# Performance work log

Measured on AMD Instinct MI355X. Metric: run time of the kernel, lower is better.

The kernel has to match this reference:

```python
import jax, jax.numpy as jnp
import numpy as np

GAMMA = 0.05
EPS = 1e-12
H, NH, HD = 768, 12, 64

def _lin(x, W, b):
    return x @ W.T + b

def _pproc(x, W, b):
    # LRP gamma-rule projection: forward value equals _lin(x, W, b); gradient flows through the gamma-modified layer times a detached ratio.
    z = _lin(x, W, b)
    zp = _lin(x, W + GAMMA * jnp.clip(W, 0.0, None), b + GAMMA * jnp.clip(b, 0.0, None))
    return zp * jax.lax.stop_gradient(z / zp)

def setup_inputs() -> dict:
    key = jax.random.key(0)
    ks = jax.random.split(key, 9)
    s = 0.02
    d = {"hidden_states": jax.random.normal(ks[0], (2, 2048, H), jnp.float32)}
    for i, n in enumerate(["q", "k", "v", "o"]):
        d["W" + n] = jax.random.normal(ks[1 + 2 * i], (H, H), jnp.float32) * s
        d["b" + n] = jax.random.normal(ks[2 + 2 * i], (H,), jnp.float32) * s
    return d

def reference(hidden_states, Wq, bq, Wk, bk, Wv, bv, Wo, bo):
    B, S, _ = hidden_states.shape
    def heads(x):  # [B,S,H] -> [B,NH,S,HD]
        return x.reshape(B, S, NH, HD).transpose(0, 2, 1, 3)
    q = heads(_pproc(hidden_states, Wq, bq))
    k = heads(_pproc(hidden_states, Wk, bk))
    v = heads(_pproc(hidden_states, Wv, bv))
    # NOTE: source has NO 1/sqrt(d_head) scaling on the scores
    scores = jnp.einsum("bhsd,bhtd->bhst", q, k)
    probs = jax.lax.stop_gradient(jax.nn.softmax(scores, axis=-1))  # detach_kq branch
    ctx = jnp.einsum("bhst,bhtd->bhsd", probs, v).transpose(0, 2, 1, 3).reshape(B, S, H)
    # BertSelfOutput.pforward: gamma-modified dense applied directly (no pproc ratio)
    pWo = Wo + GAMMA * jnp.clip(Wo, 0.0, None)
    pbo = bo + GAMMA * jnp.clip(bo, 0.0, None)
    y = _lin(ctx, pWo, pbo) + hidden_states
    # 'nowb' LayerNorm with detached mean and std (torch.std -> unbiased, ddof=1)
    mean = jax.lax.stop_gradient(jnp.mean(y, axis=-1, keepdims=True))
    std = jax.lax.stop_gradient(jnp.std(y, axis=-1, keepdims=True, ddof=1))
    out = (y - mean) / (std + EPS)
    return out, probs
```

## Files before the change

kernel.cpp:

```cpp
#include <hip/hip_runtime.h>

#define GAMMA 0.05f
#define LNEPS 1e-12f
#define HDIMT 768
#define SDIM  2048
#define NHEAD 12
#define HDHEAD 64
#define MTOT  4096
#define BHEADS 24
#define OUT0E ((size_t)MTOT * HDIMT)
#define NXEL  ((size_t)MTOT * HDIMT)
#define WNEL  ((size_t)HDIMT * HDIMT)
#define NEATT ((size_t)BHEADS * SDIM * HDHEAD)

typedef __attribute__((ext_vector_type(8))) short short8;
typedef __attribute__((ext_vector_type(4))) float f32x4;

#define MFMA16(a, b, c) __builtin_amdgcn_mfma_f32_16x16x32_bf16((a), (b), (c), 0, 0, 0)

__device__ __forceinline__ float bf2f(unsigned short u) {
    union { unsigned int i; float f; } c; c.i = ((unsigned int)u) << 16; return c.f;
}
__device__ __forceinline__ unsigned short f2bf(float f) {
    union { float f; unsigned int i; } c; c.f = f;
    unsigned int i = c.i;
    i += 0x7FFFu + ((i >> 16) & 1u);
    return (unsigned short)(i >> 16);
}
__device__ __forceinline__ void splitbf(float v, unsigned short& h, unsigned short& l) {
    h = f2bf(v);
    l = f2bf(v - bf2f(h));
}

__device__ __forceinline__ void load8f(const void* p, size_t idx, int isbf, float* r) {
    if (isbf) {
        const unsigned short* b = (const unsigned short*)p + idx;
        uint4 u = *(const uint4*)b;
        const unsigned short* pu = (const unsigned short*)&u;
        #pragma unroll
        for (int j = 0; j < 8; ++j) r[j] = bf2f(pu[j]);
    } else {
        const float* f = (const float*)p + idx;
        float4 a = *(const float4*)f, c = *(const float4*)(f + 4);
        r[0] = a.x; r[1] = a.y; r[2] = a.z; r[3] = a.w;
        r[4] = c.x; r[5] = c.y; r[6] = c.z; r[7] = c.w;
    }
}
__device__ __forceinline__ float load1f(const void* p, size_t idx, int isbf) {
    return isbf ? bf2f(((const unsigned short*)p)[idx]) : ((const float*)p)[idx];
}

__global__ void detect_kernel(const void* __restrict__ x, int* __restrict__ flag) {
    __shared__ int cnt;
    if (threadIdx.x == 0) cnt = 0;
    __syncthreads();
    const unsigned short* u = (const unsigned short*)x;
    unsigned short v = u[2 * threadIdx.x];
    int e = (v >> 7) & 0xFF;
    int ok = (e >= 100 && e <= 140) ? 1 : 0;
    atomicAdd(&cnt, ok);
    __syncthreads();
    if (threadIdx.x == 0) flag[0] = (cnt >= 192) ? 1 : 0;
}

__global__ __launch_bounds__(256) void prep_kernel(
    const void* __restrict__ x,
    const void* __restrict__ Wq, const void* __restrict__ Wk,
    const void* __restrict__ Wv, const void* __restrict__ Wo,
    unsigned short* __restrict__ xh, unsigned short* __restrict__ xl,
    unsigned short* __restrict__ wqh, unsigned short* __restrict__ wql,
    unsigned short* __restrict__ wkh, unsigned short* __restrict__ wkl,
    unsigned short* __restrict__ wvh, unsigned short* __restrict__ wvl,
    unsigned short* __restrict__ woh, unsigned short* __restrict__ wol,
    const int* __restrict__ flag)
{
    const int isbf = flag[0];
    const int z = blockIdx.y;
    const size_t i8 = ((size_t)blockIdx.x * 256 + threadIdx.x) * 8;
    const void* src; unsigned short* dh; unsigned short* dl;
    size_t n; int gam = 0;
    if (z == 0)      { src = x;  dh = xh;  dl = xl;  n = NXEL; }
    else if (z == 1) { src = Wq; dh = wqh; dl = wql; n = WNEL; }
    else if (z == 2) { src = Wk; dh = wkh; dl = wkl; n = WNEL; }
    else if (z == 3) { src = Wv; dh = wvh; dl = wvl; n = WNEL; }
    else             { src = Wo; dh = woh; dl = wol; n = WNEL; gam = 1; }
    if (i8 >= n) return;

    float v[8]; load8f(src, i8, isbf, v);
    alignas(16) unsigned short hv[8], lv[8];
    #pragma unroll
    for (int j = 0; j < 8; ++j) {
        float f = v[j];
        if (gam) f += GAMMA * fmaxf(f, 0.0f);
        splitbf(f, hv[j], lv[j]);
    }
    *(uint4*)(dh + i8) = *(const uint4*)hv;
    *(uint4*)(dl + i8) = *(const uint4*)lv;
}

#define FRAG(buf, row, kb)                                                        \
    (*(const short8*)((const char*)(buf) +                                        \
                      (((row) << 7) + ((kb) ^ (((row) & 7) << 4)))))

__global__ __launch_bounds__(256) void qkv_mfma(
    const unsigned short* __restrict__ xh, const unsigned short* __restrict__ xl,
    const unsigned short* __restrict__ wqh, const unsigned short* __restrict__ wql,
    const unsigned short* __restrict__ wkh, const unsigned short* __restrict__ wkl,
    const unsigned short* __restrict__ wvh, const unsigned short* __restrict__ wvl,
    const void* __restrict__ bq, const void* __restrict__ bk, const void* __restrict__ bv,
    unsigned short* __restrict__ qh, unsigned short* __restrict__ ql,
    unsigned short* __restrict__ kh, unsigned short* __restrict__ kl,
    unsigned short* __restrict__ vth, unsigned short* __restrict__ vtl,
    const int* __restrict__ flag)
{
    __shared__ alignas(16) unsigned short Ah[8192], Al[8192];
    __shared__ alignas(16) unsigned short Bh[4096], Bl[4096];

    const int isbf = flag[0];
    const int tid = threadIdx.x;
    const int lane = tid & 63, w = tid >> 6;
    const int l15 = lane & 15, g = lane >> 4;
    const int m0 = blockIdx.x * 128;
    const int h  = blockIdx.y;
    const int z  = blockIdx.z;

    const unsigned short* Wh = (z == 0) ? wqh : (z == 1) ? wkh : wvh;
    const unsigned short* Wl = (z == 0) ? wql : (z == 1) ? wkl : wvl;
    const void* bias = (z == 0) ? bq : (z == 1) ? bk : bv;

    f32x4 acc[2][4];
    #pragma unroll
    for (int i = 0; i < 2; ++i)
        #pragma unroll
        for (int c = 0; c < 4; ++c) acc[i][c] = (f32x4){0.0f, 0.0f, 0.0f, 0.0f};

    for (int k0 = 0; k0 < HDIMT; k0 += 64) {
        __syncthreads();
        #pragma unroll
        for (int p = 0; p < 4; ++p) {
            const int idx = tid + p * 256;
            const int row = idx >> 3, slot = idx & 7;
            const int off = (row << 7) + ((slot << 4) ^ ((row & 7) << 4));
            const size_t s = (size_t)(m0 + row) * HDIMT + k0 + slot * 8;
            *(uint4*)((char*)Ah + off) = *(const uint4*)(xh + s);
            *(uint4*)((char*)Al + off) = *(const uint4*)(xl + s);
        }
        #pragma unroll
        for (int p = 0; p < 2; ++p) {
            const int idx = tid + p * 256;
            const int row = idx >> 3, slot = idx & 7;
            const int off = (row << 7) + ((slot << 4) ^ ((row & 7) << 4));
            const size_t s = (size_t)(h * 64 + row) * HDIMT + k0 + slot * 8;
            *(uint4*)((char*)Bh + off) = *(const uint4*)(Wh + s);
            *(uint4*)((char*)Bl + off) = *(const uint4*)(Wl + s);
        }
        __syncthreads();

        #pragma unroll
        for (int ks = 0; ks < 2; ++ks) {
            const int kb = (g << 4) + (ks << 6);
            short8 a8h[2], a8l[2], b8h[4], b8l[4];
            #pragma unroll
            for (int i = 0; i < 2; ++i) {
                const int row = w * 32 + i * 16 + l15;
                a8h[i] = FRAG(Ah, row, kb);
                a8l[i] = FRAG(Al, row, kb);
            }
            #pragma unroll
            for (int c = 0; c < 4; ++c) {
                const int row = c * 16 + l15;
                b8h[c] = FRAG(Bh, row, kb);
                b8l[c] = FRAG(Bl, row, kb);
            }
            #pragma unroll
            for (int i = 0; i < 2; ++i)
                #pragma unroll
                for (int c = 0; c < 4; ++c) {
                    acc[i][c] = MFMA16(a8h[i], b8h[c], acc[i][c]);
                    acc[i][c] = MFMA16(a8l[i], b8h[c], acc[i][c]);
                    acc[i][c] = MFMA16(a8h[i], b8l[c], acc[i][c]);
                }
        }
    }

    float bb[4];
    #pragma unroll
    for (int c = 0; c < 4; ++c) bb[c] = load1f(bias, h * 64 + c * 16 + l15, isbf);

    if (z < 2) {
        unsigned short* oh = z ? kh : qh;
        unsigned short* ol = z ? kl : ql;
        #pragma unroll
        for (int i = 0; i < 2; ++i)
            #pragma unroll
            for (int c = 0; c < 4; ++c)
                #pragma unroll
                for (int r = 0; r < 4; ++r) {
                    const int m = m0 + w * 32 + i * 16 + g * 4 + r;
                    const int b = m >> 11, s = m & 2047;
                    const int d = c * 16 + l15;
                    unsigned short hu, lu;
                    splitbf(acc[i][c][r] + bb[c], hu, lu);
                    const size_t o = ((size_t)(b * NHEAD + h) * SDIM + s) * HDHEAD + d;
                    oh[o] = hu; ol[o] = lu;
                }
    } else {
        #pragma unroll
        for (int i = 0; i < 2; ++i)
            #pragma unroll
            for (int c = 0; c < 4; ++c) {
                const int m00 = m0 + w * 32 + i * 16 + g * 4;
                const int b = m00 >> 11, s0 = m00 & 2047;
                const int d = c * 16 + l15;
                ushort4 hv, lv;
                unsigned short* hp = (unsigned short*)&hv;
                unsigned short* lp = (unsigned short*)&lv;
                #pragma unroll
                for (int r = 0; r < 4; ++r)
                    splitbf(acc[i][c][r] + bb[c], hp[r], lp[r]);
                const size_t o = ((size_t)(b * NHEAD + h) * HDHEAD + d) * SDIM + s0;
                *(ushort4*)(vth + o) = hv;
                *(ushort4*)(vtl + o) = lv;
            }
    }
}

#define STAGE64(dsth, dstl, srch, srcl, SROW)                                     \
    {                                                                             \
        _Pragma("unroll")                                                         \
        for (int p_ = 0; p_ < 2; ++p_) {                                          \
            const int idx_ = tid + p_ * 256;                                      \
            const int row_ = idx_ >> 3, slot_ = idx_ & 7;                         \
            const int off_ = (row_ << 7) + ((slot_ << 4) ^ ((row_ & 7) << 4));    \
            *(uint4*)((char*)(dsth) + off_) =                                     \
                *(const uint4*)((srch) + (size_t)row_ * (SROW) + slot_ * 8);      \
            *(uint4*)((char*)(dstl) + off_) =                                     \
                *(const uint4*)((srcl) + (size_t)row_ * (SROW) + slot_ * 8);      \
        }                                                                         \
    }

__global__ __launch_bounds__(256) void attn_kernel(
    const unsigned short* __restrict__ qh, const unsigned short* __restrict__ ql,
    const unsigned short* __restrict__ kh, const unsigned short* __restrict__ kl,
    const unsigned short* __restrict__ vth, const unsigned short* __restrict__ vtl,
    unsigned short* __restrict__ ctxh, unsigned short* __restrict__ ctxl,
    void* __restrict__ dout,
    const int* __restrict__ flag)
{
    __shared__ alignas(16) unsigned short Qh[4096], Ql[4096];
    __shared__ alignas(16) unsigned short Kh[4096], Kl[4096];
    __shared__ alignas(16) unsigned short Vh[4096], Vl[4096];
    __shared__ float linv[64];

    const int isbf = flag[0];
    const int tid  = threadIdx.x;
    const int lane = tid & 63;
    const int w    = tid >> 6;
    const int l15  = lane & 15, g = lane >> 4;
    const int bh   = blockIdx.y;
    const int r0   = blockIdx.x * 64;

    {
        const unsigned short* sh = qh + ((size_t)bh * SDIM + r0) * HDHEAD;
        const unsigned short* sl = ql + ((size_t)bh * SDIM + r0) * HDHEAD;
        STAGE64(Qh, Ql, sh, sl, HDHEAD);
    }
    __syncthreads();

    short8 aqh[2], aql[2];
    #pragma unroll
    for (int ks = 0; ks < 2; ++ks) {
        const int row = w * 16 + l15;
        const int kb  = (g << 4) + (ks << 6);
        aqh[ks] = FRAG(Qh, row, kb);
        aql[ks] = FRAG(Ql, row, kb);
    }

    const f32x4 fzero = {0.0f, 0.0f, 0.0f, 0.0f};

    float lsum[4] = {0.0f, 0.0f, 0.0f, 0.0f};

    for (int kt = 0; kt < 32; ++kt) {
        __syncthreads();
        {
            const unsigned short* sh = kh + ((size_t)bh * SDIM + kt * 64) * HDHEAD;
            const unsigned short* sl = kl + ((size_t)bh * SDIM + kt * 64) * HDHEAD;
            STAGE64(Kh, Kl, sh, sl, HDHEAD);
        }
        __syncthreads();

        f32x4 acc[4];
        #pragma unroll
        for (int c = 0; c < 4; ++c) acc[c] = fzero;

        #pragma unroll
        for (int c = 0; c < 4; ++c) {
            #pragma unroll
            for (int ks = 0; ks < 2; ++ks) {
                const int row = c * 16 + l15;
                const int kb  = (g << 4) + (ks << 6);
                short8 bh8 = FRAG(Kh, row, kb);
                short8 bl8 = FRAG(Kl, row, kb);
                acc[c] = MFMA16(aqh[ks], bh8, acc[c]);
                acc[c] = MFMA16(aql[ks], bh8, acc[c]);
                acc[c] = MFMA16(aqh[ks], bl8, acc[c]);
            }
        }
        #pragma unroll
        for (int c = 0; c < 4; ++c) {
            #pragma unroll
            for (int r = 0; r < 4; ++r) lsum[r] += __expf(acc[c][r]);
        }
    }

    #pragma unroll
    for (int d = 1; d < 16; d <<= 1) {
        #pragma unroll
        for (int r = 0; r < 4; ++r) lsum[r] += __shfl_xor(lsum[r], d, 64);
    }
    #pragma unroll
    for (int r = 0; r < 4; ++r)
        if (l15 == r) linv[w * 16 + g * 4 + r] = 1.0f / lsum[r];
    __syncthreads();

    float inv[4];
    #pragma unroll
    for (int r = 0; r < 4; ++r) inv[r] = linv[w * 16 + g * 4 + r];

    f32x4 cacc[4];
    #pragma unroll
    for (int c = 0; c < 4; ++c) cacc[c] = fzero;

    for (int kt = 0; kt < 32; ++kt) {
        __syncthreads();
        {
            const unsigned short* sh = kh + ((size_t)bh * SDIM + kt * 64) * HDHEAD;
            const unsigned short* sl = kl + ((size_t)bh * SDIM + kt * 64) * HDHEAD;
            STAGE64(Kh, Kl, sh, sl, HDHEAD);
            const unsigned short* vh = vth + (size_t)bh * HDHEAD * SDIM + (size_t)(kt * 64);
            const unsigned short* vl = vtl + (size_t)bh * HDHEAD * SDIM + (size_t)(kt * 64);
            STAGE64(Vh, Vl, vh, vl, SDIM);
        }
        __syncthreads();

        f32x4 acc[4];
        #pragma unroll
        for (int c = 0; c < 4; ++c) acc[c] = fzero;

        #pragma unroll
        for (int c = 0; c < 4; ++c) {
            #pragma unroll
            for (int ks = 0; ks < 2; ++ks) {
                const int row = c * 16 + l15;
                const int kb  = (g << 4) + (ks << 6);
                short8 bh8 = FRAG(Kh, row, kb);
                short8 bl8 = FRAG(Kl, row, kb);
                acc[c] = MFMA16(aqh[ks], bh8, acc[c]);
                acc[c] = MFMA16(aql[ks], bh8, acc[c]);
                acc[c] = MFMA16(aqh[ks], bl8, acc[c]);
            }
        }
        __syncthreads();

        #pragma unroll
        for (int c = 0; c < 4; ++c) {
            const int t = c * 16 + l15;
            #pragma unroll
            for (int r = 0; r < 4; ++r) {
                const int q = w * 16 + g * 4 + r;
                const float p = __expf(acc[c][r]) * inv[r];
                const size_t go = OUT0E + ((size_t)bh * SDIM + (r0 + q)) * SDIM
                                + (size_t)(kt * 64 + t);
                if (isbf) ((unsigned short*)dout)[go] = f2bf(p);
                else      ((float*)dout)[go] = p;
                unsigned short ph_, pl_;
                splitbf(p, ph_, pl_);
                const int off = (q << 7) + ((t << 1) ^ ((q & 7) << 4));
                *(unsigned short*)((char*)Kh + off) = ph_;
                *(unsigned short*)((char*)Kl + off) = pl_;
            }
        }
        __syncthreads();

        short8 pah[2], pal[2];
        #pragma unroll
        for (int ks = 0; ks < 2; ++ks) {
            const int row = w * 16 + l15;
            const int kb  = (g << 4) + (ks << 6);
            pah[ks] = FRAG(Kh, row, kb);
            pal[ks] = FRAG(Kl, row, kb);
        }
        #pragma unroll
        for (int dsb = 0; dsb < 4; ++dsb) {
            #pragma unroll
            for (int ks = 0; ks < 2; ++ks) {
                const int row = dsb * 16 + l15;
                const int kb  = (g << 4) + (ks << 6);
                short8 vh8 = FRAG(Vh, row, kb);
                short8 vl8 = FRAG(Vl, row, kb);
                cacc[dsb] = MFMA16(pah[ks], vh8, cacc[dsb]);
                cacc[dsb] = MFMA16(pal[ks], vh8, cacc[dsb]);
                cacc[dsb] = MFMA16(pah[ks], vl8, cacc[dsb]);
            }
        }
    }

    const int bb_ = bh / NHEAD, hh_ = bh % NHEAD;
    #pragma unroll
    for (int dsb = 0; dsb < 4; ++dsb) {
        #pragma unroll
        for (int r = 0; r < 4; ++r) {
            const int q = w * 16 + g * 4 + r;
            const int d = dsb * 16 + l15;
            unsigned short hu, lu;
            splitbf(cacc[dsb][r], hu, lu);
            const size_t o = ((size_t)(bb_ * SDIM + r0 + q)) * HDIMT + hh_ * HDHEAD + d;
            ctxh[o] = hu; ctxl[o] = lu;
        }
    }
}

__global__ __launch_bounds__(256) void oproj_mfma(
    const unsigned short* __restrict__ ctxh, const unsigned short* __restrict__ ctxl,
    const unsigned short* __restrict__ woh, const unsigned short* __restrict__ wol,
    const void* __restrict__ bo, const void* __restrict__ x,
    float* __restrict__ y, const int* __restrict__ flag)
{
    __shared__ alignas(16) unsigned short Ah[8192], Al[8192];
    __shared__ alignas(16) unsigned short Bh[4096], Bl[4096];

    const int isbf = flag[0];
    const int tid = threadIdx.x;
    const int lane = tid & 63, w = tid >> 6;
    const int l15 = lane & 15, g = lane >> 4;
    const int m0 = blockIdx.x * 128;
    const int h  = blockIdx.y;

    f32x4 acc[2][4];
    #pragma unroll
    for (int i = 0; i < 2; ++i)
        #pragma unroll
        for (int c = 0; c < 4; ++c) acc[i][c] = (f32x4){0.0f, 0.0f, 0.0f, 0.0f};

    for (int k0 = 0; k0 < HDIMT; k0 += 64) {
        __syncthreads();
        #pragma unroll
        for (int p = 0; p < 4; ++p) {
            const int idx = tid + p * 256;
            const int row = idx >> 3, slot = idx & 7;
            const int off = (row << 7) + ((slot << 4) ^ ((row & 7) << 4));
            const size_t s = (size_t)(m0 + row) * HDIMT + k0 + slot * 8;
            *(uint4*)((char*)Ah + off) = *(const uint4*)(ctxh + s);
            *(uint4*)((char*)Al + off) = *(const uint4*)(ctxl + s);
        }
        #pragma unroll
        for (int p = 0; p < 2; ++p) {
            const int idx = tid + p * 256;
            const int row = idx >> 3, slot = idx & 7;
            const int off = (row << 7) + ((slot << 4) ^ ((row & 7) << 4));
            const size_t s = (size_t)(h * 64 + row) * HDIMT + k0 + slot * 8;
            *(uint4*)((char*)Bh + off) = *(const uint4*)(woh + s);
            *(uint4*)((char*)Bl + off) = *(const uint4*)(wol + s);
        }
        __syncthreads();

        #pragma unroll
        for (int ks = 0; ks < 2; ++ks) {
            const int kb = (g << 4) + (ks << 6);
            short8 a8h[2], a8l[2], b8h[4], b8l[4];
            #pragma unroll
            for (int i = 0; i < 2; ++i) {
                const int row = w * 32 + i * 16 + l15;
                a8h[i] = FRAG(Ah, row, kb);
                a8l[i] = FRAG(Al, row, kb);
            }
            #pragma unroll
            for (int c = 0; c < 4; ++c) {
                const int row = c * 16 + l15;
                b8h[c] = FRAG(Bh, row, kb);
                b8l[c] = FRAG(Bl, row, kb);
            }
            #pragma unroll
            for (int i = 0; i < 2; ++i)
                #pragma unroll
                for (int c = 0; c < 4; ++c) {
                    acc[i][c] = MFMA16(a8h[i], b8h[c], acc[i][c]);
                    acc[i][c] = MFMA16(a8l[i], b8h[c], acc[i][c]);
                    acc[i][c] = MFMA16(a8h[i], b8l[c], acc[i][c]);
                }
        }
    }

    float pb[4];
    #pragma unroll
    for (int c = 0; c < 4; ++c) {
        float t = load1f(bo, h * 64 + c * 16 + l15, isbf);
        pb[c] = t + GAMMA * fmaxf(t, 0.0f);
    }

    #pragma unroll
    for (int i = 0; i < 2; ++i)
        #pragma unroll
        for (int c = 0; c < 4; ++c)
            #pragma unroll
            for (int r = 0; r < 4; ++r) {
                const int m = m0 + w * 32 + i * 16 + g * 4 + r;
                const int n = h * 64 + c * 16 + l15;
                const size_t o = (size_t)m * HDIMT + n;
                y[o] = acc[i][c][r] + pb[c] + load1f(x, o, isbf);
            }
}

__global__ __launch_bounds__(256) void ln_kernel(
    const float* __restrict__ y, void* __restrict__ out,
    const int* __restrict__ flag)
{
    __shared__ float red[256];
    const int isbf = flag[0];
    const int m = blockIdx.x;
    const int tid = threadIdx.x;
    const float* yr = y + (size_t)m * HDIMT;

    float v0 = yr[tid], v1 = yr[tid + 256], v2 = yr[tid + 512];

    red[tid] = v0 + v1 + v2;
    __syncthreads();
    for (int s = 128; s > 0; s >>= 1) {
        if (tid < s) red[tid] += red[tid + s];
        __syncthreads();
    }
    const float mean = red[0] * (1.0f / 768.0f);
    __syncthreads();

    const float d0 = v0 - mean, d1 = v1 - mean, d2 = v2 - mean;
    red[tid] = d0 * d0 + d1 * d1 + d2 * d2;
    __syncthreads();
    for (int s = 128; s > 0; s >>= 1) {
        if (tid < s) red[tid] += red[tid + s];
        __syncthreads();
    }
    const float var = red[0] * (1.0f / 767.0f);
    const float inv = 1.0f / (sqrtf(var) + LNEPS);

    const size_t base = (size_t)m * HDIMT;
    if (isbf) {
        unsigned short* o = (unsigned short*)out;
        o[base + tid]       = f2bf(d0 * inv);
        o[base + tid + 256] = f2bf(d1 * inv);
        o[base + tid + 512] = f2bf(d2 * inv);
    } else {
        float* o = (float*)out;
        o[base + tid]       = d0 * inv;
        o[base + tid + 256] = d1 * inv;
        o[base + tid + 512] = d2 * inv;
    }
}

extern "C" void kernel_launch(void* const* d_in, const int* in_sizes, int n_in,
                              void* d_out, int out_size, void* d_ws, size_t ws_size,
                              hipStream_t stream)
{
    (void)in_sizes; (void)n_in; (void)out_size; (void)ws_size;

    const void* x  = d_in[0];
    const void* Wq = d_in[1];
    const void* bq = d_in[2];
    const void* Wk = d_in[3];
    const void* bk = d_in[4];
    const void* Wv = d_in[5];
    const void* bv = d_in[6];
    const void* Wo = d_in[7];
    const void* bo = d_in[8];

    unsigned short* qh  = (unsigned short*)d_ws;
    unsigned short* ql  = qh  + NEATT;
    unsigned short* kh  = ql  + NEATT;
    unsigned short* kl  = kh  + NEATT;
    unsigned short* vth = kl  + NEATT;
    unsigned short* vtl = vth + NEATT;
    unsigned short* xh  = vtl + NEATT;
    unsigned short* xl  = xh  + NXEL;
    unsigned short* wqh = xl  + NXEL;
    unsigned short* wql = wqh + WNEL;
    unsigned short* wkh = wql + WNEL;
    unsigned short* wkl = wkh + WNEL;
    unsigned short* wvh = wkl + WNEL;
    unsigned short* wvl = wvh + WNEL;
    unsigned short* woh = wvl + WNEL;
    unsigned short* wol = woh + WNEL;
    int* flag = (int*)(wol + WNEL);

    float* y = (float*)qh;
    unsigned short* ctxh = xh;
    unsigned short* ctxl = xl;

    detect_kernel<<<1, 256, 0, stream>>>(x, flag);
    prep_kernel<<<dim3(1536, 5), 256, 0, stream>>>(x, Wq, Wk, Wv, Wo,
                                                   xh, xl, wqh, wql, wkh, wkl,
                                                   wvh, wvl, woh, wol, flag);
    qkv_mfma<<<dim3(32, 12, 3), 256, 0, stream>>>(xh, xl, wqh, wql, wkh, wkl, wvh, wvl,
                                                  bq, bk, bv,
                                                  qh, ql, kh, kl, vth, vtl, flag);
    attn_kernel<<<dim3(32, 24), 256, 0, stream>>>(qh, ql, kh, kl, vth, vtl,
                                                  ctxh, ctxl, d_out, flag);
    oproj_mfma<<<dim3(32, 12), 256, 0, stream>>>(ctxh, ctxl, woh, wol, bo, x, y, flag);
    ln_kernel<<<MTOT, 256, 0, stream>>>(y, d_out, flag);
}
```

Before: 700.9 us.

## Use 32x32 MFMA tiles in attention, vectorize probs store, shuffle-reduce LayerNorm

Switches the attention kernel from 16x16x32 to 32x32x16 bf16 MFMA, giving each wave a 32x32 quadrant so fewer LDS fragment loads are needed per FLOP. Row sums are now combined across two waves through shared memory. The probability output is written from LDS with 16-byte vectorized, coalesced stores instead of scattered scalar stores. In the fp32 path those values are rebuilt from the hi+lo bf16 split, which may differ slightly from the exact fp32 value. LayerNorm replaces its tree reduction over shared memory with wave shuffle reductions.

```diff
diff --git a/kernel.cpp b/kernel.cpp
--- a/kernel.cpp
+++ b/kernel.cpp
@@ -15,8 +15,10 @@
 
 typedef __attribute__((ext_vector_type(8))) short short8;
 typedef __attribute__((ext_vector_type(4))) float f32x4;
+typedef __attribute__((ext_vector_type(16))) float f32x16;
 
 #define MFMA16(a, b, c) __builtin_amdgcn_mfma_f32_16x16x32_bf16((a), (b), (c), 0, 0, 0)
+#define MFMA32(a, b, c) __builtin_amdgcn_mfma_f32_32x32x16_bf16((a), (b), (c), 0, 0, 0)
 
 __device__ __forceinline__ float bf2f(unsigned short u) {
     union { unsigned int i; float f; } c; c.i = ((unsigned int)u) << 16; return c.f;
@@ -250,13 +252,16 @@
     __shared__ alignas(16) unsigned short Qh[4096], Ql[4096];
     __shared__ alignas(16) unsigned short Kh[4096], Kl[4096];
     __shared__ alignas(16) unsigned short Vh[4096], Vl[4096];
+    __shared__ float lsums[64][2];
     __shared__ float linv[64];
 
     const int isbf = flag[0];
     const int tid  = threadIdx.x;
     const int lane = tid & 63;
     const int w    = tid >> 6;
-    const int l15  = lane & 15, g = lane >> 4;
+    const int l31  = lane & 31, g2 = lane >> 5;
+    const int qh_  = (w >> 1) * 32;
+    const int th_  = (w & 1) * 32;
     const int bh   = blockIdx.y;
     const int r0   = blockIdx.x * 64;
 
@@ -267,18 +272,17 @@
     }
     __syncthreads();
 
-    short8 aqh[2], aql[2];
-    #pragma unroll
-    for (int ks = 0; ks < 2; ++ks) {
-        const int row = w * 16 + l15;
-        const int kb  = (g << 4) + (ks << 6);
-        aqh[ks] = FRAG(Qh, row, kb);
-        aql[ks] = FRAG(Ql, row, kb);
-    }
-
-    const f32x4 fzero = {0.0f, 0.0f, 0.0f, 0.0f};
-
-    float lsum[4] = {0.0f, 0.0f, 0.0f, 0.0f};
+    short8 aqh[4], aql[4];
+    #pragma unroll
+    for (int ks = 0; ks < 4; ++ks) {
+        const int kb = ks * 32 + g2 * 16;
+        aqh[ks] = FRAG(Qh, qh_ + l31, kb);
+        aql[ks] = FRAG(Ql, qh_ + l31, kb);
+    }
+
+    float lsum[16];
+    #pragma unroll
+    for (int r = 0; r < 16; ++r) lsum[r] = 0.0f;
 
     for (int kt = 0; kt < 32; ++kt) {
         __syncthreads();
@@ -289,47 +293,42 @@
         }
         __syncthreads();
 
-        f32x4 acc[4];
-        #pragma unroll
-        for (int c = 0; c < 4; ++c) acc[c] = fzero;
-
-        #pragma unroll
-        for (int c = 0; c < 4; ++c) {
-            #pragma unroll
-            for (int ks = 0; ks < 2; ++ks) {
-                const int row = c * 16 + l15;
-                const int kb  = (g << 4) + (ks << 6);
-                short8 bh8 = FRAG(Kh, row, kb);
-                short8 bl8 = FRAG(Kl, row, kb);
-                acc[c] = MFMA16(aqh[ks], bh8, acc[c]);
-                acc[c] = MFMA16(aql[ks], bh8, acc[c]);
-                acc[c] = MFMA16(aqh[ks], bl8, acc[c]);
-            }
-        }
-        #pragma unroll
-        for (int c = 0; c < 4; ++c) {
-            #pragma unroll
-            for (int r = 0; r < 4; ++r) lsum[r] += __expf(acc[c][r]);
-        }
-    }
-
-    #pragma unroll
-    for (int d = 1; d < 16; d <<= 1) {
-        #pragma unroll
-        for (int r = 0; r < 4; ++r) lsum[r] += __shfl_xor(lsum[r], d, 64);
-    }
-    #pragma unroll
-    for (int r = 0; r < 4; ++r)
-        if (l15 == r) linv[w * 16 + g * 4 + r] = 1.0f / lsum[r];
+        f32x16 acc = {};
+        #pragma unroll
+        for (int ks = 0; ks < 4; ++ks) {
+            const int kb = ks * 32 + g2 * 16;
+            short8 b8h = FRAG(Kh, th_ + l31, kb);
+            short8 b8l = FRAG(Kl, th_ + l31, kb);
+            acc = MFMA32(aqh[ks], b8h, acc);
+            acc = MFMA32(aql[ks], b8h, acc);
+            acc = MFMA32(aqh[ks], b8l, acc);
+        }
+        #pragma unroll
+        for (int r = 0; r < 16; ++r) lsum[r] += __expf(acc[r]);
+    }
+
+    #pragma unroll
+    for (int d = 1; d < 32; d <<= 1) {
+        #pragma unroll
+        for (int r = 0; r < 16; ++r) lsum[r] += __shfl_xor(lsum[r], d, 64);
+    }
+    if (l31 == 0) {
+        #pragma unroll
+        for (int r = 0; r < 16; ++r) {
+            const int qrow = qh_ + (r & 3) + 8 * (r >> 2) + 4 * g2;
+            lsums[qrow][w & 1] = lsum[r];
+        }
+    }
     __syncthreads();
-
-    float inv[4];
-    #pragma unroll
-    for (int r = 0; r < 4; ++r) inv[r] = linv[w * 16 + g * 4 + r];
-
-    f32x4 cacc[4];
-    #pragma unroll
-    for (int c = 0; c < 4; ++c) cacc[c] = fzero;
+    if (tid < 64) linv[tid] = 1.0f / (lsums[tid][0] + lsums[tid][1]);
+    __syncthreads();
+
+    float invr[16];
+    #pragma unroll
+    for (int r = 0; r < 16; ++r)
+        invr[r] = linv[qh_ + (r & 3) + 8 * (r >> 2) + 4 * g2];
+
+    f32x16 cacc = {};
 
     for (int kt = 0; kt < 32; ++kt) {
         __syncthreads();
@@ -343,80 +342,80 @@
         }
         __syncthreads();
 
-        f32x4 acc[4];
-        #pragma unroll
-        for (int c = 0; c < 4; ++c) acc[c] = fzero;
-
-        #pragma unroll
-        for (int c = 0; c < 4; ++c) {
-            #pragma unroll
-            for (int ks = 0; ks < 2; ++ks) {
-                const int row = c * 16 + l15;
-                const int kb  = (g << 4) + (ks << 6);
-                short8 bh8 = FRAG(Kh, row, kb);
-                short8 bl8 = FRAG(Kl, row, kb);
-                acc[c] = MFMA16(aqh[ks], bh8, acc[c]);
-                acc[c] = MFMA16(aql[ks], bh8, acc[c]);
-                acc[c] = MFMA16(aqh[ks], bl8, acc[c]);
+        f32x16 acc = {};
+        #pragma unroll
+        for (int ks = 0; ks < 4; ++ks) {
+            const int kb = ks * 32 + g2 * 16;
+            short8 b8h = FRAG(Kh, th_ + l31, kb);
+            short8 b8l = FRAG(Kl, th_ + l31, kb);
+            acc = MFMA32(aqh[ks], b8h, acc);
+            acc = MFMA32(aql[ks], b8h, acc);
+            acc = MFMA32(aqh[ks], b8l, acc);
+        }
+        __syncthreads();
+
+        #pragma unroll
+        for (int r = 0; r < 16; ++r) {
+            const float p = __expf(acc[r]) * invr[r];
+            const int q = qh_ + (r & 3) + 8 * (r >> 2) + 4 * g2;
+            const int t = th_ + l31;
+            unsigned short ph_, pl_;
+            splitbf(p, ph_, pl_);
+            const int off = (q << 7) + ((t << 1) ^ ((q & 7) << 4));
+            *(unsigned short*)((char*)Kh + off) = ph_;
+            *(unsigned short*)((char*)Kl + off) = pl_;
+        }
+        __syncthreads();
+
+        {
+            const int prow = tid >> 2, pt0 = (tid & 3) * 16;
+            const int swz = (prow & 7) << 4;
+            const int o0 = (prow << 7) + (((pt0 << 1) + 0) ^ swz);
+            const int o1 = (prow << 7) + (((pt0 << 1) + 16) ^ swz);
+            const size_t go = OUT0E + ((size_t)bh * SDIM + (r0 + prow)) * SDIM
+                            + (size_t)(kt * 64 + pt0);
+            uint4 h0 = *(const uint4*)((const char*)Kh + o0);
+            uint4 h1 = *(const uint4*)((const char*)Kh + o1);
+            if (isbf) {
+                *(uint4*)((unsigned short*)dout + go)     = h0;
+                *(uint4*)((unsigned short*)dout + go + 8) = h1;
+            } else {
+                uint4 l0 = *(const uint4*)((const char*)Kl + o0);
+                uint4 l1 = *(const uint4*)((const char*)Kl + o1);
+                const unsigned short* hp0 = (const unsigned short*)&h0;
+                const unsigned short* lp0 = (const unsigned short*)&l0;
+                const unsigned short* hp1 = (const unsigned short*)&h1;
+                const unsigned short* lp1 = (const unsigned short*)&l1;
+                float* op = (float*)dout + go;
+                #pragma unroll
+                for (int j = 0; j < 8; ++j) op[j]     = bf2f(hp0[j]) + bf2f(lp0[j]);
+                #pragma unroll
+                for (int j = 0; j < 8; ++j) op[8 + j] = bf2f(hp1[j]) + bf2f(lp1[j]);
             }
         }
-        __syncthreads();
-
-        #pragma unroll
-        for (int c = 0; c < 4; ++c) {
-            const int t = c * 16 + l15;
-            #pragma unroll
-            for (int r = 0; r < 4; ++r) {
-                const int q = w * 16 + g * 4 + r;
-                const float p = __expf(acc[c][r]) * inv[r];
-                const size_t go = OUT0E + ((size_t)bh * SDIM + (r0 + q)) * SDIM
-                                + (size_t)(kt * 64 + t);
-                if (isbf) ((unsigned short*)dout)[go] = f2bf(p);
-                else      ((float*)dout)[go] = p;
-                unsigned short ph_, pl_;
-                splitbf(p, ph_, pl_);
-                const int off = (q << 7) + ((t << 1) ^ ((q & 7) << 4));
-                *(unsigned short*)((char*)Kh + off) = ph_;
-                *(unsigned short*)((char*)Kl + off) = pl_;
-            }
-        }
-        __syncthreads();
-
-        short8 pah[2], pal[2];
-        #pragma unroll
-        for (int ks = 0; ks < 2; ++ks) {
-            const int row = w * 16 + l15;
-            const int kb  = (g << 4) + (ks << 6);
-            pah[ks] = FRAG(Kh, row, kb);
-            pal[ks] = FRAG(Kl, row, kb);
-        }
-        #pragma unroll
-        for (int dsb = 0; dsb < 4; ++dsb) {
-            #pragma unroll
-            for (int ks = 0; ks < 2; ++ks) {
-                const int row = dsb * 16 + l15;
-                const int kb  = (g << 4) + (ks << 6);
-                short8 vh8 = FRAG(Vh, row, kb);
-                short8 vl8 = FRAG(Vl, row, kb);
-                cacc[dsb] = MFMA16(pah[ks], vh8, cacc[dsb]);
-                cacc[dsb] = MFMA16(pal[ks], vh8, cacc[dsb]);
-                cacc[dsb] = MFMA16(pah[ks], vl8, cacc[dsb]);
-            }
+
+        #pragma unroll
+        for (int ks = 0; ks < 4; ++ks) {
+            const int kb = ks * 32 + g2 * 16;
+            short8 pah = FRAG(Kh, qh_ + l31, kb);
+            short8 pal = FRAG(Kl, qh_ + l31, kb);
+            short8 v8h = FRAG(Vh, th_ + l31, kb);
+            short8 v8l = FRAG(Vl, th_ + l31, kb);
+            cacc = MFMA32(pah, v8h, cacc);
+            cacc = MFMA32(pal, v8h, cacc);
+            cacc = MFMA32(pah, v8l, cacc);
         }
     }
 
     const int bb_ = bh / NHEAD, hh_ = bh % NHEAD;
     #pragma unroll
-    for (int dsb = 0; dsb < 4; ++dsb) {
-        #pragma unroll
-        for (int r = 0; r < 4; ++r) {
-            const int q = w * 16 + g * 4 + r;
-            const int d = dsb * 16 + l15;
-            unsigned short hu, lu;
-            splitbf(cacc[dsb][r], hu, lu);
-            const size_t o = ((size_t)(bb_ * SDIM + r0 + q)) * HDIMT + hh_ * HDHEAD + d;
-            ctxh[o] = hu; ctxl[o] = lu;
-        }
+    for (int r = 0; r < 16; ++r) {
+        const int q = qh_ + (r & 3) + 8 * (r >> 2) + 4 * g2;
+        const int d = th_ + l31;
+        unsigned short hu, lu;
+        splitbf(cacc[r], hu, lu);
+        const size_t o = ((size_t)(bb_ * SDIM + r0 + q)) * HDIMT + hh_ * HDHEAD + d;
+        ctxh[o] = hu; ctxl[o] = lu;
     }
 }
 
@@ -515,31 +514,29 @@
     const float* __restrict__ y, void* __restrict__ out,
     const int* __restrict__ flag)
 {
-    __shared__ float red[256];
+    __shared__ float part[8];
     const int isbf = flag[0];
     const int m = blockIdx.x;
     const int tid = threadIdx.x;
+    const int lane = tid & 63, w = tid >> 6;
     const float* yr = y + (size_t)m * HDIMT;
 
     float v0 = yr[tid], v1 = yr[tid + 256], v2 = yr[tid + 512];
 
-    red[tid] = v0 + v1 + v2;
+    float s = v0 + v1 + v2;
+    #pragma unroll
+    for (int d = 1; d < 64; d <<= 1) s += __shfl_xor(s, d, 64);
+    if (lane == 0) part[w] = s;
     __syncthreads();
-    for (int s = 128; s > 0; s >>= 1) {
-        if (tid < s) red[tid] += red[tid + s];
-        __syncthreads();
-    }
-    const float mean = red[0] * (1.0f / 768.0f);
+    const float mean = (part[0] + part[1] + part[2] + part[3]) * (1.0f / 768.0f);
+
+    const float d0 = v0 - mean, d1 = v1 - mean, d2 = v2 - mean;
+    float ss = d0 * d0 + d1 * d1 + d2 * d2;
+    #pragma unroll
+    for (int d = 1; d < 64; d <<= 1) ss += __shfl_xor(ss, d, 64);
+    if (lane == 0) part[4 + w] = ss;
     __syncthreads();
-
-    const float d0 = v0 - mean, d1 = v1 - mean, d2 = v2 - mean;
-    red[tid] = d0 * d0 + d1 * d1 + d2 * d2;
-    __syncthreads();
-    for (int s = 128; s > 0; s >>= 1) {
-        if (tid < s) red[tid] += red[tid + s];
-        __syncthreads();
-    }
-    const float var = red[0] * (1.0f / 767.0f);
+    const float var = (part[4] + part[5] + part[6] + part[7]) * (1.0f / 767.0f);
     const float inv = 1.0f / (sqrtf(var) + LNEPS);
 
     const size_t base = (size_t)m * HDIMT;
```

Measured after the change: 748.2 us. +6.8%, slower.
